# Kernel tuning notes

Measured on AMD Instinct MI355X. Metric: run time of the kernel, lower is better.

## Reference

```python
import jax, jax.numpy as jnp
import numpy as np

B, SQ, SK = 8, 128, 128
IVD, DIM, EV, H, NH = 32, 32, 64, 8, 128
DK = EV // H


def setup_inputs() -> dict:
    key = jax.random.key(0)
    ks = jax.random.split(key, 16)
    n = lambda k, s: jax.random.normal(k, s, dtype=jnp.float32)
    lin = lambda k, fi, fo: n(k, (fi, fo)) / np.float32(np.sqrt(fi))
    d = {}
    d['query_value'] = n(ks[0], (B, SQ, IVD))
    d['key_value']   = n(ks[1], (B, SK, IVD))
    d['value']       = n(ks[2], (B, SK, DIM))
    d['impute_data'] = n(ks[3], (B, SQ, IVD // 2))
    d['emb_mask'] = jax.random.randint(ks[4], (B, SK, DIM), 0, 2).astype(jnp.int32)
    # learn_value_embedding: Linear(IVD,NH)+Tanh+Linear(NH,EV,no bias)
    d['w1'] = lin(ks[5], IVD, NH); d['b1'] = jnp.zeros((NH,), jnp.float32)
    d['w2'] = lin(ks[6], NH, EV)
    # linears[0], linears[1]: Linear(EV,EV)
    d['wq'] = lin(ks[7], EV, EV); d['bq'] = jnp.zeros((EV,), jnp.float32)
    d['wk'] = lin(ks[8], EV, EV); d['bk'] = jnp.zeros((EV,), jnp.float32)
    # linears[2]: Linear(DIM*H, NH)
    d['wo'] = lin(ks[9], DIM * H, NH); d['bo'] = jnp.zeros((NH,), jnp.float32)
    # query_data_enc: Linear(IVD/2,NH)+LayerNorm(NH)+ReLU+Linear(NH,NH)
    d['wd1'] = lin(ks[10], IVD // 2, NH); d['bd1'] = jnp.zeros((NH,), jnp.float32)
    d['ln_g'] = jnp.ones((NH,), jnp.float32); d['ln_b'] = jnp.zeros((NH,), jnp.float32)
    d['wd2'] = lin(ks[11], NH, NH); d['bd2'] = jnp.zeros((NH,), jnp.float32)
    return d


def reference(query_value, key_value, value, impute_data,
              w1, b1, w2, wq, bq, wk, bk, wo, bo,
              wd1, bd1, ln_g, ln_b, wd2, bd2, emb_mask):
    b = query_value.shape[0]
    dim = value.shape[-1]
    # value embeddings: Linear -> Tanh -> Linear(no bias)
    qe = jnp.tanh(query_value @ w1 + b1) @ w2   # [B,Sq,EV]
    ke = jnp.tanh(key_value @ w1 + b1) @ w2     # [B,Sk,EV]
    q = (qe @ wq + bq).reshape(b, -1, H, DK).transpose(0, 2, 1, 3)  # [B,H,Sq,DK]
    k = (ke @ wk + bk).reshape(b, -1, H, DK).transpose(0, 2, 1, 3)  # [B,H,Sk,DK]
    scores = jnp.einsum('bhqd,bhkd->bhqk', q, k) / np.float32(np.sqrt(DK))
    # broadcast scores over the value channel dim; masked_fill with -10000
    m = emb_mask[:, None, None, :, :]           # [B,1,1,Sk,dim]
    logits = jnp.where(m == 0, jnp.float32(-10000.0), scores[..., None])  # [B,H,Sq,Sk,dim]
    p_attn = jax.nn.softmax(logits, axis=-2)    # softmax over Sk per channel
    out = jnp.einsum('bhqkd,bkd->bhqd', p_attn, value)  # [B,H,Sq,dim]
    x = out.transpose(0, 2, 1, 3).reshape(b, -1, H * dim)
    y = x @ wo + bo                             # [B,Sq,NH]
    # query_data_enc branch
    h1 = impute_data @ wd1 + bd1
    mu = jnp.mean(h1, axis=-1, keepdims=True)
    var = jnp.var(h1, axis=-1, keepdims=True)
    ln = (h1 - mu) / jnp.sqrt(var + 1e-5) * ln_g + ln_b
    query_data = jax.nn.relu(ln) @ wd2 + bd2    # [B,Sq,NH]
    return y, query_data
```

## Files before the change

### kernel.cpp

```cpp
#include <hip/hip_runtime.h>
#include <math.h>

#define B 8
#define SQ 128
#define SK 128
#define IVD 32
#define DIM 32
#define EV 64
#define H 8
#define NH 128
#define DK 8
#define TQ 2
#define KG 8
#define PAD 132

__device__ __forceinline__ float fast_tanh(float x) {
    const float xc = fminf(fmaxf(x, -10.f), 10.f);
    const float t = __expf(2.f * xc);
    return (t - 1.f) / (t + 1.f);
}

__global__ __launch_bounds__(128) void fused1_kernel(
    const float* __restrict__ qv, const float* __restrict__ kv,
    const float* __restrict__ w1, const float* __restrict__ b1,
    const float* __restrict__ w2,
    const float* __restrict__ wq, const float* __restrict__ bqv,
    const float* __restrict__ wk, const float* __restrict__ bkv,
    float* __restrict__ qout, float* __restrict__ kout,
    const float* __restrict__ imp,
    const float* __restrict__ wd1, const float* __restrict__ bd1,
    const float* __restrict__ ln_g, const float* __restrict__ ln_b,
    const float* __restrict__ wd2, const float* __restrict__ bd2,
    float* __restrict__ qd)
{
    const int r = blockIdx.x;
    const int tid = threadIdx.x;

    if (r < 1024) {
        __shared__ float xs[2][IVD];
        __shared__ float h1[2][NH];
        __shared__ float ev[2][EV];
        __shared__ float part[2][128];
        const float* src; const float* wp; const float* bp; float* dst;
        int row0;
        if (r < 512) { row0 = r * 2;         src = qv; wp = wq; bp = bqv; dst = qout; }
        else         { row0 = (r - 512) * 2; src = kv; wp = wk; bp = bkv; dst = kout; }

        if (tid < 2 * IVD) xs[tid >> 5][tid & 31] = src[row0 * IVD + tid];
        __syncthreads();

        {
            float a0 = b1[tid], a1 = a0;
            #pragma unroll
            for (int i = 0; i < IVD; ++i) {
                const float w = w1[i * NH + tid];
                a0 += xs[0][i] * w; a1 += xs[1][i] * w;
            }
            h1[0][tid] = fast_tanh(a0);
            h1[1][tid] = fast_tanh(a1);
        }
        __syncthreads();

        const int o = tid & 63, hf = tid >> 6;
        {
            float c0 = 0.f, c1 = 0.f;
            #pragma unroll 8
            for (int i = hf * 64; i < hf * 64 + 64; ++i) {
                const float w = w2[i * EV + o];
                c0 += h1[0][i] * w; c1 += h1[1][i] * w;
            }
            part[0][tid] = c0; part[1][tid] = c1;
        }
        __syncthreads();
        {
            const int row = tid >> 6, oo = tid & 63;
            ev[row][oo] = part[row][oo] + part[row][oo + 64];
        }
        __syncthreads();
        {
            float c0 = 0.f, c1 = 0.f;
            #pragma unroll 8
            for (int j = hf * 32; j < hf * 32 + 32; ++j) {
                const float w = wp[j * EV + o];
                c0 += ev[0][j] * w; c1 += ev[1][j] * w;
            }
            part[0][tid] = c0; part[1][tid] = c1;
        }
        __syncthreads();
        {
            const int row = tid >> 6, oo = tid & 63;
            dst[(row0 + row) * EV + oo] = part[row][oo] + part[row][oo + 64] + bp[oo];
        }
    } else {
        const int bs0 = (r - 1024) * 2;
        __shared__ float xs2[2][IVD / 2];
        __shared__ float h1b[2][NH];
        __shared__ float red[2][2];

        if (tid < IVD) xs2[tid >> 4][tid & 15] = imp[bs0 * (IVD / 2) + tid];
        __syncthreads();
        float a0 = bd1[tid], a1 = a0;
        #pragma unroll
        for (int i = 0; i < IVD / 2; ++i) {
            const float w = wd1[i * NH + tid];
            a0 += xs2[0][i] * w; a1 += xs2[1][i] * w;
        }

        float s0 = a0, s1 = a1;
        #pragma unroll
        for (int off = 32; off > 0; off >>= 1) {
            s0 += __shfl_down(s0, off, 64);
            s1 += __shfl_down(s1, off, 64);
        }
        if ((tid & 63) == 0) { red[0][tid >> 6] = s0; red[1][tid >> 6] = s1; }
        __syncthreads();
        const float mu0 = (red[0][0] + red[0][1]) * (1.f / NH);
        const float mu1 = (red[1][0] + red[1][1]) * (1.f / NH);
        const float d0 = a0 - mu0, d1 = a1 - mu1;
        float t0 = d0 * d0, t1 = d1 * d1;
        __syncthreads();
        #pragma unroll
        for (int off = 32; off > 0; off >>= 1) {
            t0 += __shfl_down(t0, off, 64);
            t1 += __shfl_down(t1, off, 64);
        }
        if ((tid & 63) == 0) { red[0][tid >> 6] = t0; red[1][tid >> 6] = t1; }
        __syncthreads();
        const float v0 = (red[0][0] + red[0][1]) * (1.f / NH);
        const float v1 = (red[1][0] + red[1][1]) * (1.f / NH);

        const float g = ln_g[tid], bb = ln_b[tid];
        h1b[0][tid] = fmaxf(d0 * rsqrtf(v0 + 1e-5f) * g + bb, 0.f);
        h1b[1][tid] = fmaxf(d1 * rsqrtf(v1 + 1e-5f) * g + bb, 0.f);
        __syncthreads();

        float c0 = bd2[tid], c1 = c0;
        #pragma unroll 8
        for (int j = 0; j < NH; ++j) {
            const float w = wd2[j * NH + tid];
            c0 += h1b[0][j] * w; c1 += h1b[1][j] * w;
        }
        qd[bs0 * NH + tid] = c0;
        qd[(bs0 + 1) * NH + tid] = c1;
    }
}

__global__ __launch_bounds__(256) void attn_kernel(
    const float* __restrict__ qproj, const float* __restrict__ kproj,
    const float* __restrict__ value, const int* __restrict__ mask,
    const float* __restrict__ wo, const float* __restrict__ bo,
    float* __restrict__ y)
{
    const int blk = blockIdx.x;
    const int b = blk >> 6;
    const int q0 = (blk & 63) * TQ;
    const int tid = threadIdx.x;

    __shared__ __align__(16) float qs[TQ * EV];
    __shared__ __align__(16) float sc[TQ * H * SK];
    __shared__ __align__(16) float mvt[DIM * PAD];
    __shared__ __align__(16) float mmt[DIM * PAD];
    __shared__ __align__(16) float2 part[H * KG * DIM];
    __shared__ __align__(16) float xr[TQ * H * DIM];
    __shared__ __align__(16) float ypart[2 * TQ * NH];

    if (tid < TQ * EV) qs[tid] = qproj[(b * SQ + q0) * EV + tid] * 0.3535533905932738f;
    for (int idx = tid; idx < SK * DIM; idx += 256) {
        const int k = idx >> 5, d = idx & 31;
        const float v = value[b * SK * DIM + idx];
        const float m = (float)mask[b * SK * DIM + idx];
        mvt[d * PAD + k] = v * m;
        mmt[d * PAD + k] = m;
    }
    __syncthreads();

    #pragma unroll
    for (int i = 0; i < (TQ * H * SK) / 256; ++i) {
        const int p = tid + i * 256;
        const int q = p >> 10, rem = p & 1023, h = rem >> 7, k = rem & 127;
        const float4* kr = (const float4*)(kproj + (b * SK + k) * EV + h * DK);
        const float4* qq = (const float4*)(qs + q * EV + h * DK);
        const float4 k0 = kr[0], k1 = kr[1], qa = qq[0], qb = qq[1];
        const float s = qa.x * k0.x + qa.y * k0.y + qa.z * k0.z + qa.w * k0.w
                      + qb.x * k1.x + qb.y * k1.y + qb.z * k1.z + qb.w * k1.w;
        sc[p] = __expf(s);
    }
    __syncthreads();

    {
        const int d = tid & 31, kg = tid >> 5;
        float4 vv[4], mq[4];
        const float4* vp = (const float4*)&mvt[d * PAD + kg * 16];
        const float4* mp = (const float4*)&mmt[d * PAD + kg * 16];
        #pragma unroll
        for (int j = 0; j < 4; ++j) { vv[j] = vp[j]; mq[j] = mp[j]; }

        #pragma unroll
        for (int q = 0; q < TQ; ++q) {
            #pragma unroll
            for (int h = 0; h < H; ++h) {
                const float4* sp = (const float4*)&sc[(q * H + h) * SK + kg * 16];
                float num = 0.f, den = 0.f;
                #pragma unroll
                for (int j = 0; j < 4; ++j) {
                    const float4 s = sp[j];
                    num += s.x * vv[j].x + s.y * vv[j].y + s.z * vv[j].z + s.w * vv[j].w;
                    den += s.x * mq[j].x + s.y * mq[j].y + s.z * mq[j].z + s.w * mq[j].w;
                }
                part[(h * KG + kg) * DIM + d] = make_float2(num, den);
            }
            __syncthreads();
            {
                const int h = tid >> 5;
                float num = 0.f, den = 0.f;
                #pragma unroll
                for (int g = 0; g < KG; ++g) {
                    const float2 p2 = part[(h * KG + g) * DIM + d];
                    num += p2.x; den += p2.y;
                }
                xr[q * (H * DIM) + tid] = num / den;
            }
            __syncthreads();
        }
    }

    {
        const int n = tid & 127, half = tid >> 7;
        const float* wop = wo + half * 128 * NH + n;
        const float* x0 = xr + half * 128;
        const float* x1 = xr + (H * DIM) + half * 128;
        float a0 = 0.f, a1 = 0.f;
        #pragma unroll 4
        for (int j = 0; j < 128; ++j) {
            const float w = wop[j * NH];
            a0 += w * x0[j];
            a1 += w * x1[j];
        }
        ypart[half * (TQ * NH) + 0 * NH + n] = a0;
        ypart[half * (TQ * NH) + 1 * NH + n] = a1;
    }
    __syncthreads();
    {
        const int q = tid >> 7, n = tid & 127;
        y[(b * SQ + q0 + q) * NH + n] =
            ypart[q * NH + n] + ypart[TQ * NH + q * NH + n] + bo[n];
    }
}

extern "C" void kernel_launch(void* const* d_in, const int* in_sizes, int n_in,
                              void* d_out, int out_size, void* d_ws, size_t ws_size,
                              hipStream_t stream) {
    const float* query_value = (const float*)d_in[0];
    const float* key_value   = (const float*)d_in[1];
    const float* value       = (const float*)d_in[2];
    const float* impute      = (const float*)d_in[3];
    const int*   emb_mask    = (const int*)d_in[4];
    const float* w1   = (const float*)d_in[5];
    const float* b1   = (const float*)d_in[6];
    const float* w2   = (const float*)d_in[7];
    const float* wq   = (const float*)d_in[8];
    const float* bq   = (const float*)d_in[9];
    const float* wk   = (const float*)d_in[10];
    const float* bk   = (const float*)d_in[11];
    const float* wo   = (const float*)d_in[12];
    const float* bo   = (const float*)d_in[13];
    const float* wd1  = (const float*)d_in[14];
    const float* bd1  = (const float*)d_in[15];
    const float* ln_g = (const float*)d_in[16];
    const float* ln_b = (const float*)d_in[17];
    const float* wd2  = (const float*)d_in[18];
    const float* bd2  = (const float*)d_in[19];

    float* y  = (float*)d_out;
    float* qd = y + B * SQ * NH;

    float* qproj = (float*)d_ws;
    float* kproj = qproj + B * SQ * EV;

    hipLaunchKernelGGL(fused1_kernel, dim3(1536), dim3(128), 0, stream,
                       query_value, key_value, w1, b1, w2, wq, bq, wk, bk,
                       qproj, kproj,
                       impute, wd1, bd1, ln_g, ln_b, wd2, bd2, qd);
    hipLaunchKernelGGL(attn_kernel, dim3(B * SQ / TQ), dim3(256), 0, stream,
                       qproj, kproj, value, emb_mask, wo, bo, y);
}
```

Before: 115.3 us.

## Fuse query projection and impute encoder into attention kernel, one query per block

Moves the query embedding and projection, plus the impute-data encoder, into the attention kernel. Two 128-thread teams compute these side by side, and each block now handles a single query row (1024 blocks). The first kernel now only computes key projections, and the mask is read directly into registers instead of being staged in a second shared-memory array. The aim is to drop the q-projection round trip through global memory and shrink shared memory to raise occupancy. In exchange, value and mask staging is now repeated per query rather than per pair of queries, which doubles that redundant global traffic.

After: 120.9 us. 4.9% more time.

```diff
diff --git a/kernel.cpp b/kernel.cpp
--- a/kernel.cpp
+++ b/kernel.cpp
@@ -10,7 +10,6 @@
 #define H 8
 #define NH 128
 #define DK 8
-#define TQ 2
 #define KG 8
 #define PAD 132
 
@@ -20,231 +19,243 @@
     return (t - 1.f) / (t + 1.f);
 }
 
-__global__ __launch_bounds__(128) void fused1_kernel(
-    const float* __restrict__ qv, const float* __restrict__ kv,
+__global__ __launch_bounds__(128) void kproj_kernel(
+    const float* __restrict__ kv,
+    const float* __restrict__ w1, const float* __restrict__ b1,
+    const float* __restrict__ w2,
+    const float* __restrict__ wk, const float* __restrict__ bkv,
+    float* __restrict__ kout)
+{
+    const int r = blockIdx.x;
+    const int tid = threadIdx.x;
+    const int row0 = r * 2;
+
+    __shared__ float xs[2][IVD];
+    __shared__ float h1[2][NH];
+    __shared__ float ev[2][EV];
+    __shared__ float part[2][128];
+
+    if (tid < 2 * IVD) xs[tid >> 5][tid & 31] = kv[row0 * IVD + tid];
+    __syncthreads();
+
+    {
+        float a0 = b1[tid], a1 = a0;
+        #pragma unroll
+        for (int i = 0; i < IVD; ++i) {
+            const float w = w1[i * NH + tid];
+            a0 += xs[0][i] * w; a1 += xs[1][i] * w;
+        }
+        h1[0][tid] = fast_tanh(a0);
+        h1[1][tid] = fast_tanh(a1);
+    }
+    __syncthreads();
+
+    const int o = tid & 63, hf = tid >> 6;
+    {
+        float c0 = 0.f, c1 = 0.f;
+        #pragma unroll 8
+        for (int i = hf * 64; i < hf * 64 + 64; ++i) {
+            const float w = w2[i * EV + o];
+            c0 += h1[0][i] * w; c1 += h1[1][i] * w;
+        }
+        part[0][tid] = c0; part[1][tid] = c1;
+    }
+    __syncthreads();
+    {
+        const int row = tid >> 6, oo = tid & 63;
+        ev[row][oo] = part[row][oo] + part[row][oo + 64];
+    }
+    __syncthreads();
+    {
+        float c0 = 0.f, c1 = 0.f;
+        #pragma unroll 8
+        for (int j = hf * 32; j < hf * 32 + 32; ++j) {
+            const float w = wk[j * EV + o];
+            c0 += ev[0][j] * w; c1 += ev[1][j] * w;
+        }
+        part[0][tid] = c0; part[1][tid] = c1;
+    }
+    __syncthreads();
+    {
+        const int row = tid >> 6, oo = tid & 63;
+        kout[(row0 + row) * EV + oo] = part[row][oo] + part[row][oo + 64] + bkv[oo];
+    }
+}
+
+__global__ __launch_bounds__(256, 4) void attn_kernel(
+    const float* __restrict__ qv, const float* __restrict__ kproj,
+    const float* __restrict__ value, const int* __restrict__ mask,
+    const float* __restrict__ imp,
     const float* __restrict__ w1, const float* __restrict__ b1,
     const float* __restrict__ w2,
     const float* __restrict__ wq, const float* __restrict__ bqv,
-    const float* __restrict__ wk, const float* __restrict__ bkv,
-    float* __restrict__ qout, float* __restrict__ kout,
-    const float* __restrict__ imp,
+    const float* __restrict__ wo, const float* __restrict__ bo,
     const float* __restrict__ wd1, const float* __restrict__ bd1,
     const float* __restrict__ ln_g, const float* __restrict__ ln_b,
     const float* __restrict__ wd2, const float* __restrict__ bd2,
-    float* __restrict__ qd)
-{
-    const int r = blockIdx.x;
-    const int tid = threadIdx.x;
-
-    if (r < 1024) {
-        __shared__ float xs[2][IVD];
-        __shared__ float h1[2][NH];
-        __shared__ float ev[2][EV];
-        __shared__ float part[2][128];
-        const float* src; const float* wp; const float* bp; float* dst;
-        int row0;
-        if (r < 512) { row0 = r * 2;         src = qv; wp = wq; bp = bqv; dst = qout; }
-        else         { row0 = (r - 512) * 2; src = kv; wp = wk; bp = bkv; dst = kout; }
-
-        if (tid < 2 * IVD) xs[tid >> 5][tid & 31] = src[row0 * IVD + tid];
-        __syncthreads();
-
-        {
-            float a0 = b1[tid], a1 = a0;
-            #pragma unroll
-            for (int i = 0; i < IVD; ++i) {
-                const float w = w1[i * NH + tid];
-                a0 += xs[0][i] * w; a1 += xs[1][i] * w;
-            }
-            h1[0][tid] = fast_tanh(a0);
-            h1[1][tid] = fast_tanh(a1);
-        }
-        __syncthreads();
-
-        const int o = tid & 63, hf = tid >> 6;
-        {
-            float c0 = 0.f, c1 = 0.f;
-            #pragma unroll 8
-            for (int i = hf * 64; i < hf * 64 + 64; ++i) {
-                const float w = w2[i * EV + o];
-                c0 += h1[0][i] * w; c1 += h1[1][i] * w;
-            }
-            part[0][tid] = c0; part[1][tid] = c1;
-        }
-        __syncthreads();
-        {
-            const int row = tid >> 6, oo = tid & 63;
-            ev[row][oo] = part[row][oo] + part[row][oo + 64];
-        }
-        __syncthreads();
-        {
-            float c0 = 0.f, c1 = 0.f;
-            #pragma unroll 8
-            for (int j = hf * 32; j < hf * 32 + 32; ++j) {
-                const float w = wp[j * EV + o];
-                c0 += ev[0][j] * w; c1 += ev[1][j] * w;
-            }
-            part[0][tid] = c0; part[1][tid] = c1;
-        }
-        __syncthreads();
-        {
-            const int row = tid >> 6, oo = tid & 63;
-            dst[(row0 + row) * EV + oo] = part[row][oo] + part[row][oo + 64] + bp[oo];
-        }
-    } else {
-        const int bs0 = (r - 1024) * 2;
-        __shared__ float xs2[2][IVD / 2];
-        __shared__ float h1b[2][NH];
-        __shared__ float red[2][2];
-
-        if (tid < IVD) xs2[tid >> 4][tid & 15] = imp[bs0 * (IVD / 2) + tid];
-        __syncthreads();
-        float a0 = bd1[tid], a1 = a0;
-        #pragma unroll
-        for (int i = 0; i < IVD / 2; ++i) {
-            const float w = wd1[i * NH + tid];
-            a0 += xs2[0][i] * w; a1 += xs2[1][i] * w;
-        }
-
-        float s0 = a0, s1 = a1;
-        #pragma unroll
-        for (int off = 32; off > 0; off >>= 1) {
-            s0 += __shfl_down(s0, off, 64);
-            s1 += __shfl_down(s1, off, 64);
-        }
-        if ((tid & 63) == 0) { red[0][tid >> 6] = s0; red[1][tid >> 6] = s1; }
-        __syncthreads();
-        const float mu0 = (red[0][0] + red[0][1]) * (1.f / NH);
-        const float mu1 = (red[1][0] + red[1][1]) * (1.f / NH);
-        const float d0 = a0 - mu0, d1 = a1 - mu1;
-        float t0 = d0 * d0, t1 = d1 * d1;
-        __syncthreads();
-        #pragma unroll
-        for (int off = 32; off > 0; off >>= 1) {
-            t0 += __shfl_down(t0, off, 64);
-            t1 += __shfl_down(t1, off, 64);
-        }
-        if ((tid & 63) == 0) { red[0][tid >> 6] = t0; red[1][tid >> 6] = t1; }
-        __syncthreads();
-        const float v0 = (red[0][0] + red[0][1]) * (1.f / NH);
-        const float v1 = (red[1][0] + red[1][1]) * (1.f / NH);
-
-        const float g = ln_g[tid], bb = ln_b[tid];
-        h1b[0][tid] = fmaxf(d0 * rsqrtf(v0 + 1e-5f) * g + bb, 0.f);
-        h1b[1][tid] = fmaxf(d1 * rsqrtf(v1 + 1e-5f) * g + bb, 0.f);
-        __syncthreads();
-
-        float c0 = bd2[tid], c1 = c0;
-        #pragma unroll 8
-        for (int j = 0; j < NH; ++j) {
-            const float w = wd2[j * NH + tid];
-            c0 += h1b[0][j] * w; c1 += h1b[1][j] * w;
-        }
-        qd[bs0 * NH + tid] = c0;
-        qd[(bs0 + 1) * NH + tid] = c1;
-    }
-}
-
-__global__ __launch_bounds__(256) void attn_kernel(
-    const float* __restrict__ qproj, const float* __restrict__ kproj,
-    const float* __restrict__ value, const int* __restrict__ mask,
-    const float* __restrict__ wo, const float* __restrict__ bo,
-    float* __restrict__ y)
+    float* __restrict__ y, float* __restrict__ qd)
 {
     const int blk = blockIdx.x;
-    const int b = blk >> 6;
-    const int q0 = (blk & 63) * TQ;
+    const int b = blk >> 7;
     const int tid = threadIdx.x;
-
-    __shared__ __align__(16) float qs[TQ * EV];
-    __shared__ __align__(16) float sc[TQ * H * SK];
+    const int team = tid >> 7;
+    const int t = tid & 127;
+
+    __shared__ __align__(16) float qs[EV];
+    __shared__ __align__(16) float sc[H * SK];
     __shared__ __align__(16) float mvt[DIM * PAD];
-    __shared__ __align__(16) float mmt[DIM * PAD];
-    __shared__ __align__(16) float2 part[H * KG * DIM];
-    __shared__ __align__(16) float xr[TQ * H * DIM];
-    __shared__ __align__(16) float ypart[2 * TQ * NH];
-
-    if (tid < TQ * EV) qs[tid] = qproj[(b * SQ + q0) * EV + tid] * 0.3535533905932738f;
+    __shared__ __align__(16) float2 part[4 * KG * DIM];
+    __shared__ __align__(16) float xr[H * DIM];
+    __shared__ __align__(16) float ypart[2][NH];
+    __shared__ float xs[IVD];
+    __shared__ float h1[NH];
+    __shared__ float ev[EV];
+    __shared__ float pPA[128];
+    __shared__ float xs2[IVD / 2];
+    __shared__ float h1b[NH];
+    __shared__ float redm[2], redv[2];
+
+    const int d = tid & 31, kg = tid >> 5;
+
     for (int idx = tid; idx < SK * DIM; idx += 256) {
-        const int k = idx >> 5, d = idx & 31;
-        const float v = value[b * SK * DIM + idx];
-        const float m = (float)mask[b * SK * DIM + idx];
-        mvt[d * PAD + k] = v * m;
-        mmt[d * PAD + k] = m;
-    }
-    __syncthreads();
+        const int k = idx >> 5, dd = idx & 31;
+        mvt[dd * PAD + k] = value[b * SK * DIM + idx] * (float)mask[b * SK * DIM + idx];
+    }
+    if (team == 0) { if (t < IVD)     xs[t]  = qv[blk * IVD + t]; }
+    else           { if (t < IVD / 2) xs2[t] = imp[blk * (IVD / 2) + t]; }
+    __syncthreads();
+
+    float impA = 0.f;
+    if (team == 0) {
+        float a = b1[t];
+        #pragma unroll
+        for (int i = 0; i < IVD; ++i) a += xs[i] * w1[i * NH + t];
+        h1[t] = fast_tanh(a);
+    } else {
+        float a = bd1[t];
+        #pragma unroll
+        for (int i = 0; i < IVD / 2; ++i) a += xs2[i] * wd1[i * NH + t];
+        impA = a;
+        float s = a;
+        #pragma unroll
+        for (int off = 32; off > 0; off >>= 1) s += __shfl_down(s, off, 64);
+        if ((t & 63) == 0) redm[t >> 6] = s;
+    }
+    __syncthreads();
+
+    float impD = 0.f;
+    if (team == 0) {
+        const int o = t & 63, hf = t >> 6;
+        float c = 0.f;
+        #pragma unroll 8
+        for (int i = hf * 64; i < hf * 64 + 64; ++i) c += h1[i] * w2[i * EV + o];
+        pPA[t] = c;
+    } else {
+        const float mu = (redm[0] + redm[1]) * (1.f / NH);
+        impD = impA - mu;
+        float v2 = impD * impD;
+        #pragma unroll
+        for (int off = 32; off > 0; off >>= 1) v2 += __shfl_down(v2, off, 64);
+        if ((t & 63) == 0) redv[t >> 6] = v2;
+    }
+    __syncthreads();
+
+    if (team == 0) {
+        if (t < EV) ev[t] = pPA[t] + pPA[t + 64];
+    } else {
+        const float var = (redv[0] + redv[1]) * (1.f / NH);
+        h1b[t] = fmaxf(impD * rsqrtf(var + 1e-5f) * ln_g[t] + ln_b[t], 0.f);
+    }
+    __syncthreads();
+
+    if (team == 0) {
+        const int o = t & 63, hf = t >> 6;
+        float c = 0.f;
+        #pragma unroll 8
+        for (int j = hf * 32; j < hf * 32 + 32; ++j) c += ev[j] * wq[j * EV + o];
+        pPA[t] = c;
+    } else {
+        float c = bd2[t];
+        #pragma unroll 8
+        for (int j = 0; j < NH; ++j) c += h1b[j] * wd2[j * NH + t];
+        qd[blk * NH + t] = c;
+    }
+    __syncthreads();
+
+    if (team == 0 && t < EV)
+        qs[t] = (pPA[t] + pPA[t + 64] + bqv[t]) * 0.3535533905932738f;
+    __syncthreads();
+
+    float4 mq[4];
+    {
+        const int* mb = mask + b * SK * DIM + d;
+        #pragma unroll
+        for (int j = 0; j < 4; ++j) {
+            const int k0 = kg * 16 + j * 4;
+            mq[j] = make_float4((float)mb[(k0 + 0) * DIM], (float)mb[(k0 + 1) * DIM],
+                                (float)mb[(k0 + 2) * DIM], (float)mb[(k0 + 3) * DIM]);
+        }
+    }
 
     #pragma unroll
-    for (int i = 0; i < (TQ * H * SK) / 256; ++i) {
+    for (int i = 0; i < (H * SK) / 256; ++i) {
         const int p = tid + i * 256;
-        const int q = p >> 10, rem = p & 1023, h = rem >> 7, k = rem & 127;
+        const int h = p >> 7, k = p & 127;
         const float4* kr = (const float4*)(kproj + (b * SK + k) * EV + h * DK);
-        const float4* qq = (const float4*)(qs + q * EV + h * DK);
+        const float4* qq = (const float4*)(qs + h * DK);
         const float4 k0 = kr[0], k1 = kr[1], qa = qq[0], qb = qq[1];
-        const float s = qa.x * k0.x + qa.y * k0.y + qa.z * k0.z + qa.w * k0.w
-                      + qb.x * k1.x + qb.y * k1.y + qb.z * k1.z + qb.w * k1.w;
-        sc[p] = __expf(s);
-    }
-    __syncthreads();
-
-    {
-        const int d = tid & 31, kg = tid >> 5;
-        float4 vv[4], mq[4];
+        sc[p] = __expf(qa.x * k0.x + qa.y * k0.y + qa.z * k0.z + qa.w * k0.w
+                     + qb.x * k1.x + qb.y * k1.y + qb.z * k1.z + qb.w * k1.w);
+    }
+    __syncthreads();
+
+    float4 vv[4];
+    {
         const float4* vp = (const float4*)&mvt[d * PAD + kg * 16];
-        const float4* mp = (const float4*)&mmt[d * PAD + kg * 16];
-        #pragma unroll
-        for (int j = 0; j < 4; ++j) { vv[j] = vp[j]; mq[j] = mp[j]; }
-
-        #pragma unroll
-        for (int q = 0; q < TQ; ++q) {
+        #pragma unroll
+        for (int j = 0; j < 4; ++j) vv[j] = vp[j];
+    }
+    #pragma unroll
+    for (int hp = 0; hp < 2; ++hp) {
+        #pragma unroll
+        for (int hl = 0; hl < 4; ++hl) {
+            const int h = hp * 4 + hl;
+            const float4* sp = (const float4*)&sc[h * SK + kg * 16];
+            float num = 0.f, den = 0.f;
             #pragma unroll
-            for (int h = 0; h < H; ++h) {
-                const float4* sp = (const float4*)&sc[(q * H + h) * SK + kg * 16];
-                float num = 0.f, den = 0.f;
-                #pragma unroll
-                for (int j = 0; j < 4; ++j) {
-                    const float4 s = sp[j];
-                    num += s.x * vv[j].x + s.y * vv[j].y + s.z * vv[j].z + s.w * vv[j].w;
-                    den += s.x * mq[j].x + s.y * mq[j].y + s.z * mq[j].z + s.w * mq[j].w;
-                }
-                part[(h * KG + kg) * DIM + d] = make_float2(num, den);
+            for (int j = 0; j < 4; ++j) {
+                const float4 s = sp[j];
+                num += s.x * vv[j].x + s.y * vv[j].y + s.z * vv[j].z + s.w * vv[j].w;
+                den += s.x * mq[j].x + s.y * mq[j].y + s.z * mq[j].z + s.w * mq[j].w;
             }
-            __syncthreads();
-            {
-                const int h = tid >> 5;
-                float num = 0.f, den = 0.f;
-                #pragma unroll
-                for (int g = 0; g < KG; ++g) {
-                    const float2 p2 = part[(h * KG + g) * DIM + d];
-                    num += p2.x; den += p2.y;
-                }
-                xr[q * (H * DIM) + tid] = num / den;
+            part[(hl * KG + kg) * DIM + d] = make_float2(num, den);
+        }
+        __syncthreads();
+        if (kg < 4) {
+            const int hl = kg;
+            float num = 0.f, den = 0.f;
+            #pragma unroll
+            for (int g = 0; g < KG; ++g) {
+                const float2 p2 = part[(hl * KG + g) * DIM + d];
+                num += p2.x; den += p2.y;
             }
-            __syncthreads();
-        }
-    }
-
-    {
-        const int n = tid & 127, half = tid >> 7;
-        const float* wop = wo + half * 128 * NH + n;
-        const float* x0 = xr + half * 128;
-        const float* x1 = xr + (H * DIM) + half * 128;
-        float a0 = 0.f, a1 = 0.f;
+            xr[(hp * 4 + hl) * DIM + d] = num / den;
+        }
+        __syncthreads();
+    }
+
+    {
+        const int n = tid & 127, hh = tid >> 7;
+        const float* wop = wo + hh * 128 * NH + n;
+        const float* x0 = xr + hh * 128;
+        float a = 0.f;
         #pragma unroll 4
-        for (int j = 0; j < 128; ++j) {
-            const float w = wop[j * NH];
-            a0 += w * x0[j];
-            a1 += w * x1[j];
-        }
-        ypart[half * (TQ * NH) + 0 * NH + n] = a0;
-        ypart[half * (TQ * NH) + 1 * NH + n] = a1;
-    }
-    __syncthreads();
-    {
-        const int q = tid >> 7, n = tid & 127;
-        y[(b * SQ + q0 + q) * NH + n] =
-            ypart[q * NH + n] + ypart[TQ * NH + q * NH + n] + bo[n];
-    }
+        for (int j = 0; j < 128; ++j) a += wop[j * NH] * x0[j];
+        ypart[hh][n] = a;
+    }
+    __syncthreads();
+    if (tid < NH)
+        y[blk * NH + tid] = ypart[0][tid] + ypart[1][tid] + bo[tid];
 }
 
 extern "C" void kernel_launch(void* const* d_in, const int* in_sizes, int n_in,
@@ -274,13 +285,12 @@
     float* y  = (float*)d_out;
     float* qd = y + B * SQ * NH;
 
-    float* qproj = (float*)d_ws;
-    float* kproj = qproj + B * SQ * EV;
-
-    hipLaunchKernelGGL(fused1_kernel, dim3(1536), dim3(128), 0, stream,
-                       query_value, key_value, w1, b1, w2, wq, bq, wk, bk,
-                       qproj, kproj,
-                       impute, wd1, bd1, ln_g, ln_b, wd2, bd2, qd);
-    hipLaunchKernelGGL(attn_kernel, dim3(B * SQ / TQ), dim3(256), 0, stream,
-                       qproj, kproj, value, emb_mask, wo, bo, y);
-}
+    float* kproj = (float*)d_ws;
+
+    hipLaunchKernelGGL(kproj_kernel, dim3(B * SK / 2), dim3(128), 0, stream,
+                       key_value, w1, b1, w2, wk, bk, kproj);
+    hipLaunchKernelGGL(attn_kernel, dim3(B * SQ), dim3(256), 0, stream,
+                       query_value, kproj, value, emb_mask, impute,
+                       w1, b1, w2, wq, bq, wo, bo,
+                       wd1, bd1, ln_g, ln_b, wd2, bd2, y, qd);
+}
```

## Load masked value directly into registers and double attn block threads

Applied to the files above, without the earlier changes.

The attention kernel stops staging the masked value and mask tiles through transposed shared memory. Each thread now loads its strided value/mask column straight from global memory into registers. The block grows to 512 threads so both query rows are processed at once, which removes the per-query sync loop, and the output projection is split into four K-quarters. Shared memory use drops and occupancy can rise, at the cost of uncoalesced strided global loads of value and mask (redundant across the two query halves).

Measured after the change: 113.3 us (median of 2 runs). About the same (-1.7%).

```diff
diff --git a/kernel.cpp b/kernel.cpp
--- a/kernel.cpp
+++ b/kernel.cpp
@@ -12,7 +12,6 @@
 #define DK 8
 #define TQ 2
 #define KG 8
-#define PAD 132
 
 __device__ __forceinline__ float fast_tanh(float x) {
     const float xc = fminf(fmaxf(x, -10.f), 10.f);
@@ -145,7 +144,7 @@
     }
 }
 
-__global__ __launch_bounds__(256) void attn_kernel(
+__global__ __launch_bounds__(512, 4) void attn_kernel(
     const float* __restrict__ qproj, const float* __restrict__ kproj,
     const float* __restrict__ value, const int* __restrict__ mask,
     const float* __restrict__ wo, const float* __restrict__ bo,
@@ -158,25 +157,37 @@
 
     __shared__ __align__(16) float qs[TQ * EV];
     __shared__ __align__(16) float sc[TQ * H * SK];
-    __shared__ __align__(16) float mvt[DIM * PAD];
-    __shared__ __align__(16) float mmt[DIM * PAD];
-    __shared__ __align__(16) float2 part[H * KG * DIM];
+    __shared__ __align__(16) float2 part[TQ * H * KG * DIM];
     __shared__ __align__(16) float xr[TQ * H * DIM];
-    __shared__ __align__(16) float ypart[2 * TQ * NH];
+    __shared__ __align__(16) float ypart[4][TQ * NH];
+
+    const int d = tid & 31, kg = (tid >> 5) & 7, qh = tid >> 8;
+
+    float4 vv[4], mq[4];
+    {
+        const float* vb = value + b * SK * DIM + d;
+        const int*   mb = mask  + b * SK * DIM + d;
+        #pragma unroll
+        for (int j = 0; j < 4; ++j) {
+            const int k0 = kg * 16 + j * 4;
+            const float m0 = (float)mb[(k0 + 0) * DIM];
+            const float m1 = (float)mb[(k0 + 1) * DIM];
+            const float m2 = (float)mb[(k0 + 2) * DIM];
+            const float m3 = (float)mb[(k0 + 3) * DIM];
+            mq[j] = make_float4(m0, m1, m2, m3);
+            vv[j] = make_float4(vb[(k0 + 0) * DIM] * m0,
+                                vb[(k0 + 1) * DIM] * m1,
+                                vb[(k0 + 2) * DIM] * m2,
+                                vb[(k0 + 3) * DIM] * m3);
+        }
+    }
 
     if (tid < TQ * EV) qs[tid] = qproj[(b * SQ + q0) * EV + tid] * 0.3535533905932738f;
-    for (int idx = tid; idx < SK * DIM; idx += 256) {
-        const int k = idx >> 5, d = idx & 31;
-        const float v = value[b * SK * DIM + idx];
-        const float m = (float)mask[b * SK * DIM + idx];
-        mvt[d * PAD + k] = v * m;
-        mmt[d * PAD + k] = m;
-    }
     __syncthreads();
 
     #pragma unroll
-    for (int i = 0; i < (TQ * H * SK) / 256; ++i) {
-        const int p = tid + i * 256;
+    for (int i = 0; i < (TQ * H * SK) / 512; ++i) {
+        const int p = tid + i * 512;
         const int q = p >> 10, rem = p & 1023, h = rem >> 7, k = rem & 127;
         const float4* kr = (const float4*)(kproj + (b * SK + k) * EV + h * DK);
         const float4* qq = (const float4*)(qs + q * EV + h * DK);
@@ -187,63 +198,52 @@
     }
     __syncthreads();
 
+    #pragma unroll
+    for (int h = 0; h < H; ++h) {
+        const float4* sp = (const float4*)&sc[(qh * H + h) * SK + kg * 16];
+        float num = 0.f, den = 0.f;
+        #pragma unroll
+        for (int j = 0; j < 4; ++j) {
+            const float4 s = sp[j];
+            num += s.x * vv[j].x + s.y * vv[j].y + s.z * vv[j].z + s.w * vv[j].w;
+            den += s.x * mq[j].x + s.y * mq[j].y + s.z * mq[j].z + s.w * mq[j].w;
+        }
+        part[((qh * H + h) * KG + kg) * DIM + d] = make_float2(num, den);
+    }
+    __syncthreads();
     {
-        const int d = tid & 31, kg = tid >> 5;
-        float4 vv[4], mq[4];
-        const float4* vp = (const float4*)&mvt[d * PAD + kg * 16];
-        const float4* mp = (const float4*)&mmt[d * PAD + kg * 16];
-        #pragma unroll
-        for (int j = 0; j < 4; ++j) { vv[j] = vp[j]; mq[j] = mp[j]; }
-
-        #pragma unroll
-        for (int q = 0; q < TQ; ++q) {
-            #pragma unroll
-            for (int h = 0; h < H; ++h) {
-                const float4* sp = (const float4*)&sc[(q * H + h) * SK + kg * 16];
-                float num = 0.f, den = 0.f;
-                #pragma unroll
-                for (int j = 0; j < 4; ++j) {
-                    const float4 s = sp[j];
-                    num += s.x * vv[j].x + s.y * vv[j].y + s.z * vv[j].z + s.w * vv[j].w;
-                    den += s.x * mq[j].x + s.y * mq[j].y + s.z * mq[j].z + s.w * mq[j].w;
-                }
-                part[(h * KG + kg) * DIM + d] = make_float2(num, den);
-            }
-            __syncthreads();
-            {
-                const int h = tid >> 5;
-                float num = 0.f, den = 0.f;
-                #pragma unroll
-                for (int g = 0; g < KG; ++g) {
-                    const float2 p2 = part[(h * KG + g) * DIM + d];
-                    num += p2.x; den += p2.y;
-                }
-                xr[q * (H * DIM) + tid] = num / den;
-            }
-            __syncthreads();
-        }
-    }
+        const int h2 = (tid >> 5) & 7;
+        float num = 0.f, den = 0.f;
+        #pragma unroll
+        for (int g = 0; g < KG; ++g) {
+            const float2 p2 = part[((qh * H + h2) * KG + g) * DIM + d];
+            num += p2.x; den += p2.y;
+        }
+        xr[qh * (H * DIM) + h2 * DIM + d] = num / den;
+    }
+    __syncthreads();
 
     {
-        const int n = tid & 127, half = tid >> 7;
-        const float* wop = wo + half * 128 * NH + n;
-        const float* x0 = xr + half * 128;
-        const float* x1 = xr + (H * DIM) + half * 128;
+        const int n = tid & 127, quarter = tid >> 7;
+        const float* wop = wo + quarter * 64 * NH + n;
+        const float* x0 = xr + quarter * 64;
+        const float* x1 = xr + (H * DIM) + quarter * 64;
         float a0 = 0.f, a1 = 0.f;
         #pragma unroll 4
-        for (int j = 0; j < 128; ++j) {
+        for (int j = 0; j < 64; ++j) {
             const float w = wop[j * NH];
             a0 += w * x0[j];
             a1 += w * x1[j];
         }
-        ypart[half * (TQ * NH) + 0 * NH + n] = a0;
-        ypart[half * (TQ * NH) + 1 * NH + n] = a1;
-    }
-    __syncthreads();
-    {
+        ypart[quarter][0 * NH + n] = a0;
+        ypart[quarter][1 * NH + n] = a1;
+    }
+    __syncthreads();
+    if (tid < TQ * NH) {
         const int q = tid >> 7, n = tid & 127;
         y[(b * SQ + q0 + q) * NH + n] =
-            ypart[q * NH + n] + ypart[TQ * NH + q * NH + n] + bo[n];
+            (ypart[0][q * NH + n] + ypart[1][q * NH + n])
+          + (ypart[2][q * NH + n] + ypart[3][q * NH + n]) + bo[n];
     }
 }
 
@@ -281,6 +281,6 @@
                        query_value, key_value, w1, b1, w2, wq, bq, wk, bk,
                        qproj, kproj,
                        impute, wd1, bd1, ln_g, ln_b, wd2, bd2, qd);
-    hipLaunchKernelGGL(attn_kernel, dim3(B * SQ / TQ), dim3(256), 0, stream,
+    hipLaunchKernelGGL(attn_kernel, dim3(B * SQ / TQ), dim3(512), 0, stream,
                        qproj, kproj, value, emb_mask, wo, bo, y);
 }
```
